# Performance work log

Hardware: AMD Instinct MI355X
Metric: run time of the kernel (lower is better)

The kernel has to match this reference:

```python
import jax, jax.numpy as jnp
import numpy as np
from jax import lax

B, W_LEN, V, E, C, K, L = 8, 1000, 50000, 100, 50, 3, 18000


def setup_inputs() -> dict:
    key = jax.random.key(0)
    ks = jax.random.split(key, 7)
    return {
        "x": jax.random.randint(ks[0], (B, W_LEN), 0, V),
        "W_embed": jax.random.normal(ks[1], (V, E), dtype=jnp.float32) * 0.1,
        "conv_w": jax.random.normal(ks[2], (C, E, K), dtype=jnp.float32) * 0.08,
        "conv_b": jax.random.normal(ks[3], (C,), dtype=jnp.float32) * 0.01,
        "u_w": jax.random.normal(ks[4], (L, C), dtype=jnp.float32) * 0.1,
        "out_w": jax.random.normal(ks[5], (L, C), dtype=jnp.float32) * 0.1,
        "out_b": jax.random.normal(ks[6], (L,), dtype=jnp.float32) * 0.01,
    }


def reference(x, W_embed, conv_w, conv_b, u_w, out_w, out_b):
    # embedding lookup: (B, W, E)
    emb = W_embed[x]
    # conv1d over sequence, 'same' padding: (B, C, W)
    emb_ncw = jnp.transpose(emb, (0, 2, 1))
    H = lax.conv_general_dilated(
        emb_ncw, conv_w, window_strides=(1,), padding=[(K // 2, K // 2)],
        dimension_numbers=("NCH", "OIH", "NCH"))
    H = jnp.tanh(H + conv_b[None, :, None])
    H = jnp.transpose(H, (0, 2, 1))  # (B, W, C)
    # label-wise attention scores: (B, L, W), softmax over seq
    scores = jnp.einsum("lc,bwc->blw", u_w, H)
    attns = jax.nn.softmax(scores, axis=2)
    # attention-pooled reps: (B, L, C)
    m = jnp.einsum("blw,bwc->blc", attns, H)
    # per-label weighted dot product + bias, sigmoid: (B, L)
    out = jax.nn.sigmoid(jnp.sum(out_w[None] * m, axis=2) + out_b[None])
    return out
```

## Files before the change

### kernel.cpp

```cpp
#include <hip/hip_runtime.h>
#include <hip/hip_bf16.h>
#include <cmath>

#define AS1 __attribute__((address_space(1)))
#define AS3 __attribute__((address_space(3)))

#define B_ 8
#define W_LEN_ 1000
#define WP 1024
#define E_ 100
#define C_ 50
#define CPAD 64
#define HP 72
#define K_ 3
#define L_ 18000
#define TL 128
#define NLBLK ((L_ + TL - 1) / TL)
#define CWT 16
#define NSLOT (K_ * (E_ / 4))

typedef __attribute__((ext_vector_type(8))) short bf16x8;
typedef __attribute__((ext_vector_type(4))) short bf16x4;
typedef __attribute__((ext_vector_type(4))) float f32x4;

static __device__ __forceinline__ void gl_lds16(const void* g, void* l) {
    __builtin_amdgcn_global_load_lds((const AS1 unsigned*)g, (AS3 unsigned*)l, 16, 0, 0);
}
static __device__ __forceinline__ float bf2f(short s) {
    return __uint_as_float(((unsigned)(unsigned short)s) << 16);
}

__global__ __launch_bounds__(256) void prep_all(
    const float* __restrict__ conv_w, const float* __restrict__ u_w,
    const float* __restrict__ out_w,
    bf16x4* __restrict__ cwTs, __hip_bfloat16* __restrict__ UO)
{
    int tid = blockIdx.x * blockDim.x + threadIdx.x;
    if (tid < NSLOT * C_) {
        int slot = tid / C_;
        int c    = tid % C_;
        int k = slot / (E_ / 4);
        int i = slot % (E_ / 4);
        bf16x4 v;
        #pragma unroll
        for (int q = 0; q < 4; q++) {
            __hip_bfloat16 h = __float2bfloat16(conv_w[((size_t)c * E_ + 4 * i + q) * K_ + k]);
            v[q] = *reinterpret_cast<short*>(&h);
        }
        cwTs[tid] = v;
    }
    if (tid < 2 * L_ * CPAD) {
        int c = tid & (CPAD - 1);
        int l = (tid >> 6) % L_;
        int m = tid / (L_ * CPAD);
        const float* src = m ? out_w : u_w;
        float v = (c < C_) ? src[(size_t)l * C_ + c] : 0.f;
        UO[tid] = __float2bfloat16(v);
    }
}

__global__ __launch_bounds__(256) void conv_kernel(
    const int* __restrict__ x,
    const float* __restrict__ W_embed,
    const bf16x4* __restrict__ cwTs,
    const float* __restrict__ conv_b,
    __hip_bfloat16* __restrict__ H)
{
    __shared__ float4 emb_s[(CWT + 2) * (E_ / 4)];
    __shared__ bf16x4 wS[NSLOT * C_];

    const int b  = blockIdx.y;
    const int w0 = blockIdx.x * CWT;
    const int tid = threadIdx.x;

    for (int i = tid; i < NSLOT * C_; i += 256) wS[i] = cwTs[i];

    for (int i = tid; i < (CWT + 2) * (E_ / 4); i += 256) {
        int row = i / (E_ / 4);
        int e4  = i % (E_ / 4);
        int ws  = w0 - 1 + row;
        float4 v = make_float4(0.f, 0.f, 0.f, 0.f);
        if ((unsigned)ws < (unsigned)W_LEN_)
            v = ((const float4*)(W_embed + (size_t)x[b * W_LEN_ + ws] * E_))[e4];
        emb_s[i] = v;
    }
    __syncthreads();

    const int c  = tid & 63;
    const int wq = tid >> 6;
    const int cc = (c < C_) ? c : 0;

    f32x4 acc[4];
    const float bias = conv_b[cc];
    #pragma unroll
    for (int j = 0; j < 4; j++) acc[j] = (f32x4){bias, 0.f, 0.f, 0.f};

    const float4* eb = &emb_s[wq * 4 * (E_ / 4)];

    #pragma unroll 5
    for (int i = 0; i < E_ / 4; i++) {
        bf16x4 kb0 = wS[i * C_ + cc];
        bf16x4 kb1 = wS[(25 + i) * C_ + cc];
        bf16x4 kb2 = wS[(50 + i) * C_ + cc];
        float4 k0 = make_float4(bf2f(kb0[0]), bf2f(kb0[1]), bf2f(kb0[2]), bf2f(kb0[3]));
        float4 k1 = make_float4(bf2f(kb1[0]), bf2f(kb1[1]), bf2f(kb1[2]), bf2f(kb1[3]));
        float4 k2 = make_float4(bf2f(kb2[0]), bf2f(kb2[1]), bf2f(kb2[2]), bf2f(kb2[3]));
        float4 e0 = eb[i],       e1 = eb[25 + i],  e2 = eb[50 + i];
        float4 e3 = eb[75 + i],  e4 = eb[100 + i], e5 = eb[125 + i];
        acc[0].x += e0.x*k0.x + e1.x*k1.x + e2.x*k2.x;
        acc[0].y += e0.y*k0.y + e1.y*k1.y + e2.y*k2.y;
        acc[0].z += e0.z*k0.z + e1.z*k1.z + e2.z*k2.z;
        acc[0].w += e0.w*k0.w + e1.w*k1.w + e2.w*k2.w;
        acc[1].x += e1.x*k0.x + e2.x*k1.x + e3.x*k2.x;
        acc[1].y += e1.y*k0.y + e2.y*k1.y + e3.y*k2.y;
        acc[1].z += e1.z*k0.z + e2.z*k1.z + e3.z*k2.z;
        acc[1].w += e1.w*k0.w + e2.w*k1.w + e3.w*k2.w;
        acc[2].x += e2.x*k0.x + e3.x*k1.x + e4.x*k2.x;
        acc[2].y += e2.y*k0.y + e3.y*k1.y + e4.y*k2.y;
        acc[2].z += e2.z*k0.z + e3.z*k1.z + e4.z*k2.z;
        acc[2].w += e2.w*k0.w + e3.w*k1.w + e4.w*k2.w;
        acc[3].x += e3.x*k0.x + e4.x*k1.x + e5.x*k2.x;
        acc[3].y += e3.y*k0.y + e4.y*k1.y + e5.y*k2.y;
        acc[3].z += e3.z*k0.z + e4.z*k1.z + e5.z*k2.z;
        acc[3].w += e3.w*k0.w + e4.w*k1.w + e5.w*k2.w;
    }

    #pragma unroll
    for (int j = 0; j < 4; j++) {
        int w = w0 + wq * 4 + j;
        float v = 0.f;
        if (c < C_ && w < W_LEN_)
            v = tanhf((acc[j].x + acc[j].z) + (acc[j].y + acc[j].w));
        __hip_bfloat16* row = H + ((size_t)b * WP + w) * HP;
        row[c] = __float2bfloat16(v);
        if (c < HP - 64) row[64 + c] = __float2bfloat16(0.f);
    }
}

__global__ __launch_bounds__(256) void attn_kernel(
    const __hip_bfloat16* __restrict__ H,
    const __hip_bfloat16* __restrict__ UO,
    const float* __restrict__ out_b,
    float* __restrict__ out)
{
    __shared__ __hip_bfloat16 Hs[2][64 * HP];

    const int b  = blockIdx.y;
    const int l0 = blockIdx.x * TL;
    const int tid  = threadIdx.x;
    const int lane = tid & 63;
    const int wid  = tid >> 6;
    const int col = lane & 15, quad = lane >> 4;

    bf16x8 Uf[2][2], Of[2][2];
    #pragma unroll
    for (int mt = 0; mt < 2; mt++) {
        int l = l0 + wid * 32 + mt * 16 + col;
        if (l >= L_) l = L_ - 1;
        const __hip_bfloat16* up = UO + (size_t)l * CPAD + quad * 8;
        const __hip_bfloat16* op = up + (size_t)L_ * CPAD;
        #pragma unroll
        for (int st = 0; st < 2; st++) {
            Uf[mt][st] = *(const bf16x8*)(up + st * 32);
            Of[mt][st] = *(const bf16x8*)(op + st * 32);
        }
    }

    f32x4 lsum[2] = {{0.f,0.f,0.f,0.f},{0.f,0.f,0.f,0.f}};
    f32x4 num [2] = {{0.f,0.f,0.f,0.f},{0.f,0.f,0.f,0.f}};
    const f32x4 zero = {0.f, 0.f, 0.f, 0.f};

    const __hip_bfloat16* Hb = H + (size_t)b * WP * HP;

    {
        const char* g = (const char*)Hb;
        char* l = (char*)&Hs[0][0];
        gl_lds16(g + tid * 16,         l + tid * 16);
        gl_lds16(g + (tid + 256) * 16, l + (tid + 256) * 16);
        if (tid < 64)
            gl_lds16(g + (tid + 512) * 16, l + (tid + 512) * 16);
    }

    #pragma unroll 2
    for (int wt = 0; wt < WP; wt += 64) {
        const int cur = (wt >> 6) & 1;
        __syncthreads();

        if (wt + 64 < WP) {
            const char* g = (const char*)(Hb + (size_t)(wt + 64) * HP);
            char* l = (char*)&Hs[cur ^ 1][0];
            gl_lds16(g + tid * 16,         l + tid * 16);
            gl_lds16(g + (tid + 256) * 16, l + (tid + 256) * 16);
            if (tid < 64)
                gl_lds16(g + (tid + 512) * 16, l + (tid + 512) * 16);
        }

        bf16x8 Bc[4][2];
        #pragma unroll
        for (int nt = 0; nt < 4; nt++)
            #pragma unroll
            for (int st = 0; st < 2; st++)
                Bc[nt][st] = *(const bf16x8*)(&Hs[cur][(nt * 16 + col) * HP
                                                       + quad * 8 + st * 32]);

        #pragma unroll
        for (int nt = 0; nt < 4; nt++) {
            #pragma unroll
            for (int mt = 0; mt < 2; mt++) {
                f32x4 S = __builtin_amdgcn_mfma_f32_16x16x32_bf16(Uf[mt][0], Bc[nt][0], zero, 0, 0, 0);
                S       = __builtin_amdgcn_mfma_f32_16x16x32_bf16(Uf[mt][1], Bc[nt][1], S,    0, 0, 0);
                f32x4 T = __builtin_amdgcn_mfma_f32_16x16x32_bf16(Of[mt][0], Bc[nt][0], zero, 0, 0, 0);
                T       = __builtin_amdgcn_mfma_f32_16x16x32_bf16(Of[mt][1], Bc[nt][1], T,    0, 0, 0);
                #pragma unroll
                for (int r = 0; r < 4; r++) {
                    float p = __expf(S[r]);
                    lsum[mt][r] += p;
                    num [mt][r] += p * T[r];
                }
            }
        }
    }

    #pragma unroll
    for (int mt = 0; mt < 2; mt++) {
        #pragma unroll
        for (int r = 0; r < 4; r++) {
            float ls = lsum[mt][r], nm = num[mt][r];
            #pragma unroll
            for (int d = 1; d < 16; d <<= 1) {
                ls += __shfl_xor(ls, d, 64);
                nm += __shfl_xor(nm, d, 64);
            }
            if (col == 0) {
                int l = l0 + wid * 32 + mt * 16 + quad * 4 + r;
                if (l < L_) {
                    float z = nm / (ls - (float)(WP - W_LEN_)) + out_b[l];
                    out[(size_t)b * L_ + l] = 1.f / (1.f + __expf(-z));
                }
            }
        }
    }
}

extern "C" void kernel_launch(void* const* d_in, const int* in_sizes, int n_in,
                              void* d_out, int out_size, void* d_ws, size_t ws_size,
                              hipStream_t stream) {
    const int*   x       = (const int*)  d_in[0];
    const float* W_embed = (const float*)d_in[1];
    const float* conv_w  = (const float*)d_in[2];
    const float* conv_b  = (const float*)d_in[3];
    const float* u_w     = (const float*)d_in[4];
    const float* out_w   = (const float*)d_in[5];
    const float* out_b   = (const float*)d_in[6];
    float* out = (float*)d_out;

    char* ws = (char*)d_ws;
    __hip_bfloat16* H  = (__hip_bfloat16*)ws;
    __hip_bfloat16* UO = (__hip_bfloat16*)(ws + 1179648);
    bf16x4*       cwTs = (bf16x4*)(ws + 1179648 + 4608000);

    {
        const int total = 2 * L_ * CPAD;
        prep_all<<<dim3((total + 255) / 256), 256, 0, stream>>>(conv_w, u_w, out_w, cwTs, UO);
    }
    {
        dim3 grid(WP / CWT, B_);
        conv_kernel<<<grid, 256, 0, stream>>>(x, W_embed, cwTs, conv_b, H);
    }
    {
        dim3 grid(NLBLK, B_);
        attn_kernel<<<grid, 256, 0, stream>>>(H, UO, out_b, out);
    }
}
```

Measured before the change: 155.9 us.

## Split attention block across label and sequence halves with wider W tiles

```diff
diff --git a/kernel.cpp b/kernel.cpp
--- a/kernel.cpp
+++ b/kernel.cpp
@@ -14,8 +14,9 @@
 #define HP 72
 #define K_ 3
 #define L_ 18000
-#define TL 128
+#define TL 64
 #define NLBLK ((L_ + TL - 1) / TL)
+#define WTILE 128
 #define CWT 16
 #define NSLOT (K_ * (E_ / 4))
 
@@ -143,19 +144,21 @@
     const float* __restrict__ out_b,
     float* __restrict__ out)
 {
-    __shared__ __hip_bfloat16 Hs[2][64 * HP];
+    __shared__ __hip_bfloat16 Hs[2][WTILE * HP];
+    __shared__ float2 red[2][TL];
 
     const int b  = blockIdx.y;
     const int l0 = blockIdx.x * TL;
     const int tid  = threadIdx.x;
     const int lane = tid & 63;
     const int wid  = tid >> 6;
+    const int mi = wid & 1, ni = wid >> 1;
     const int col = lane & 15, quad = lane >> 4;
 
     bf16x8 Uf[2][2], Of[2][2];
     #pragma unroll
     for (int mt = 0; mt < 2; mt++) {
-        int l = l0 + wid * 32 + mt * 16 + col;
+        int l = l0 + mi * 32 + mt * 16 + col;
         if (l >= L_) l = L_ - 1;
         const __hip_bfloat16* up = UO + (size_t)l * CPAD + quad * 8;
         const __hip_bfloat16* op = up + (size_t)L_ * CPAD;
@@ -172,50 +175,56 @@
 
     const __hip_bfloat16* Hb = H + (size_t)b * WP * HP;
 
-    {
-        const char* g = (const char*)Hb;
-        char* l = (char*)&Hs[0][0];
-        gl_lds16(g + tid * 16,         l + tid * 16);
-        gl_lds16(g + (tid + 256) * 16, l + (tid + 256) * 16);
-        if (tid < 64)
-            gl_lds16(g + (tid + 512) * 16, l + (tid + 512) * 16);
-    }
-
-    #pragma unroll 2
-    for (int wt = 0; wt < WP; wt += 64) {
-        const int cur = (wt >> 6) & 1;
+    #define STAGE(buf, tile)                                                        \
+    {                                                                               \
+        const char* g = (const char*)(Hb + (size_t)(tile) * WTILE * HP);            \
+        char* l = (char*)&Hs[buf][0];                                               \
+        gl_lds16(g + tid * 16,          l + tid * 16);                              \
+        gl_lds16(g + (tid + 256) * 16,  l + (tid + 256) * 16);                      \
+        gl_lds16(g + (tid + 512) * 16,  l + (tid + 512) * 16);                      \
+        gl_lds16(g + (tid + 768) * 16,  l + (tid + 768) * 16);                      \
+        if (tid < 128)                                                              \
+            gl_lds16(g + (tid + 1024) * 16, l + (tid + 1024) * 16);                 \
+    }
+
+    STAGE(0, 0)
+
+    #pragma unroll 1
+    for (int t = 0; t < WP / WTILE; t++) {
+        const int cur = t & 1;
         __syncthreads();
 
-        if (wt + 64 < WP) {
-            const char* g = (const char*)(Hb + (size_t)(wt + 64) * HP);
-            char* l = (char*)&Hs[cur ^ 1][0];
-            gl_lds16(g + tid * 16,         l + tid * 16);
-            gl_lds16(g + (tid + 256) * 16, l + (tid + 256) * 16);
-            if (tid < 64)
-                gl_lds16(g + (tid + 512) * 16, l + (tid + 512) * 16);
-        }
-
-        bf16x8 Bc[4][2];
-        #pragma unroll
-        for (int nt = 0; nt < 4; nt++)
+        if (t + 1 < WP / WTILE)
+            STAGE(cur ^ 1, t + 1)
+
+        #pragma unroll
+        for (int half = 0; half < 2; half++) {
+            const __hip_bfloat16* Hc = &Hs[cur][half * 64 * HP];
+
+            bf16x8 Bc[2][2];
             #pragma unroll
-            for (int st = 0; st < 2; st++)
-                Bc[nt][st] = *(const bf16x8*)(&Hs[cur][(nt * 16 + col) * HP
-                                                       + quad * 8 + st * 32]);
-
-        #pragma unroll
-        for (int nt = 0; nt < 4; nt++) {
+            for (int nt = 0; nt < 2; nt++)
+                #pragma unroll
+                for (int st = 0; st < 2; st++)
+                    Bc[nt][st] = *(const bf16x8*)(&Hc[(ni * 32 + nt * 16 + col) * HP
+                                                      + quad * 8 + st * 32]);
+
             #pragma unroll
-            for (int mt = 0; mt < 2; mt++) {
-                f32x4 S = __builtin_amdgcn_mfma_f32_16x16x32_bf16(Uf[mt][0], Bc[nt][0], zero, 0, 0, 0);
-                S       = __builtin_amdgcn_mfma_f32_16x16x32_bf16(Uf[mt][1], Bc[nt][1], S,    0, 0, 0);
-                f32x4 T = __builtin_amdgcn_mfma_f32_16x16x32_bf16(Of[mt][0], Bc[nt][0], zero, 0, 0, 0);
-                T       = __builtin_amdgcn_mfma_f32_16x16x32_bf16(Of[mt][1], Bc[nt][1], T,    0, 0, 0);
+            for (int nt = 0; nt < 2; nt++) {
                 #pragma unroll
-                for (int r = 0; r < 4; r++) {
-                    float p = __expf(S[r]);
-                    lsum[mt][r] += p;
-                    num [mt][r] += p * T[r];
+                for (int mt = 0; mt < 2; mt++) {
+                    __builtin_amdgcn_s_setprio(1);
+                    f32x4 S = __builtin_amdgcn_mfma_f32_16x16x32_bf16(Uf[mt][0], Bc[nt][0], zero, 0, 0, 0);
+                    S       = __builtin_amdgcn_mfma_f32_16x16x32_bf16(Uf[mt][1], Bc[nt][1], S,    0, 0, 0);
+                    f32x4 T = __builtin_amdgcn_mfma_f32_16x16x32_bf16(Of[mt][0], Bc[nt][0], zero, 0, 0, 0);
+                    T       = __builtin_amdgcn_mfma_f32_16x16x32_bf16(Of[mt][1], Bc[nt][1], T,    0, 0, 0);
+                    __builtin_amdgcn_s_setprio(0);
+                    #pragma unroll
+                    for (int r = 0; r < 4; r++) {
+                        float p = __expf(S[r]);
+                        lsum[mt][r] += p;
+                        num [mt][r] += p * T[r];
+                    }
                 }
             }
         }
@@ -231,13 +240,18 @@
                 ls += __shfl_xor(ls, d, 64);
                 nm += __shfl_xor(nm, d, 64);
             }
-            if (col == 0) {
-                int l = l0 + wid * 32 + mt * 16 + quad * 4 + r;
-                if (l < L_) {
-                    float z = nm / (ls - (float)(WP - W_LEN_)) + out_b[l];
-                    out[(size_t)b * L_ + l] = 1.f / (1.f + __expf(-z));
-                }
-            }
+            if (col == 0)
+                red[ni][mi * 32 + mt * 16 + quad * 4 + r] = make_float2(ls, nm);
+        }
+    }
+    __syncthreads();
+
+    if (tid < TL) {
+        int l = l0 + tid;
+        if (l < L_) {
+            float2 p0 = red[0][tid], p1 = red[1][tid];
+            float z = (p0.y + p1.y) / (p0.x + p1.x - (float)(WP - W_LEN_)) + out_b[l];
+            out[(size_t)b * L_ + l] = 1.f / (1.f + __expf(-z));
         }
     }
 }
```

New measurement: 149.7 us. 1.04x faster.
